# Performance work log

Hardware: AMD Instinct MI355X
Metric: run time of the kernel (lower is better)

Reference implementation:

```python
import jax, jax.numpy as jnp
import numpy as np

B, S, DIM = 32, 1, 2048
N_HEADS, N_KV = 32, 8
HEAD_DIM = DIM // N_HEADS  # 64
MAXB, MAXS = 32, 2048
START_POS = 2047
THETA = 10000.0  # precompute_freqs_cis called without theta -> llama default


def setup_inputs() -> dict:
    key = jax.random.key(0)
    ks = jax.random.split(key, 7)
    u = lambda k, s: jax.random.uniform(k, s, jnp.float32) * 0.02  # scaled torch.rand init
    return {
        "x": jax.random.normal(ks[0], (B, S, DIM), jnp.float32),
        "q_w": u(ks[1], (DIM, N_HEADS * HEAD_DIM)),
        "k_w": u(ks[2], (DIM, N_KV * HEAD_DIM)),
        "v_w": u(ks[3], (DIM, N_KV * HEAD_DIM)),
        "o_w": u(ks[4], (DIM, N_HEADS * HEAD_DIM)),
        "cache_k": jax.random.normal(ks[5], (MAXB, MAXS, N_KV, HEAD_DIM), jnp.float32) * 0.02,
        "cache_v": jax.random.normal(ks[6], (MAXB, MAXS, N_KV, HEAD_DIM), jnp.float32) * 0.02,
        "start_pos": START_POS,
    }


def _rope(x, cos, sin):
    # x: [B, S, H, D]; consecutive pairs (even, odd) form complex numbers (llama view_as_complex)
    xr, xi = x[..., 0::2], x[..., 1::2]
    out = jnp.stack([xr * cos - xi * sin, xr * sin + xi * cos], axis=-1)
    return out.reshape(x.shape)


def _attn_fwd(x, q_w, k_w, v_w, o_w, cache_k, cache_v, start_pos):
    B_, S_, _ = x.shape
    # fused_linear(x, W) == x @ W
    xq = (x @ q_w).reshape(B_, S_, N_HEADS, HEAD_DIM)
    xk = (x @ k_w).reshape(B_, S_, N_KV, HEAD_DIM)
    xv = (x @ v_w).reshape(B_, S_, N_KV, HEAD_DIM)

    # RoPE freqs for positions [start_pos, start_pos + S)
    inv = 1.0 / (THETA ** (jnp.arange(0, HEAD_DIM, 2, dtype=jnp.float32) / HEAD_DIM))
    t = jnp.arange(start_pos, start_pos + S_, dtype=jnp.float32)
    ang = t[:, None] * inv[None, :]                    # [S, D/2]
    cos = jnp.cos(ang)[None, :, None, :]               # [1, S, 1, D/2]
    sin = jnp.sin(ang)[None, :, None, :]
    xq = _rope(xq, cos, sin)
    xk = _rope(xk, cos, sin)

    # KV-cache append
    cache_k = jax.lax.dynamic_update_slice(cache_k, xk, (0, start_pos, 0, 0))
    cache_v = jax.lax.dynamic_update_slice(cache_v, xv, (0, start_pos, 0, 0))
    L = start_pos + S_
    keys = cache_k[:B_, :L].transpose(0, 2, 1, 3)      # [B, Hkv, L, D]
    vals = cache_v[:B_, :L].transpose(0, 2, 1, 3)

    # GQA attention; grouped einsum = repeat_kv without materializing copies
    rep = N_HEADS // N_KV
    q = xq.transpose(0, 2, 1, 3).reshape(B_, N_KV, rep, S_, HEAD_DIM)
    scores = jnp.einsum('bkrsd,bkld->bkrsl', q, keys) * (HEAD_DIM ** -0.5)
    p = jax.nn.softmax(scores, axis=-1)
    o = jnp.einsum('bkrsl,bkld->bkrsd', p, vals)
    o = o.reshape(B_, N_HEADS, S_, HEAD_DIM).transpose(0, 2, 1, 3).reshape(B_, S_, -1)
    return o @ o_w


def reference(x, q_w, k_w, v_w, o_w, cache_k, cache_v, start_pos):
    return _attn_fwd(x, q_w, k_w, v_w, o_w, cache_k, cache_v, start_pos)
```

## Files before the change

kernel.cpp:

```cpp
#include <hip/hip_runtime.h>
#include <hip/hip_bf16.h>
#include <math.h>

#define NQKV 3072
#define NS 8
#define SPL 256

__device__ __forceinline__ int read_sp(const int* spp) {
  if (!spp) return 2047;
  int raw = spp[0];
  if (raw >= 0 && raw < 2048) return raw;
  union { int i; float f; } u; u.i = raw;
  if (u.f >= 0.f && u.f < 2048.f) return (int)u.f;
  return 2047;
}

__global__ __launch_bounds__(256) void k_prep(const float* __restrict__ x,
                                              float* __restrict__ xt,
                                              float* __restrict__ rope,
                                              const int* __restrict__ spp) {
  int idx = blockIdx.x * 256 + threadIdx.x;
  int r = idx >> 11, k = idx & 2047;
  xt[k * 32 + r] = x[idx];
  if (blockIdx.x == 0 && threadIdx.x < 32) {
    int i = threadIdx.x;
    int sp = read_sp(spp);
    double freq = pow(10000.0, -(double)(2 * i) / 64.0);
    double ang = (double)sp * freq;
    double sd, cd; sincos(ang, &sd, &cd);
    rope[2 * i]     = (float)cd;
    rope[2 * i + 1] = (float)sd;
  }
}

__global__ __launch_bounds__(256) void k_qkv(const float* __restrict__ qw,
                                             const float* __restrict__ kw,
                                             const float* __restrict__ vw,
                                             const float* __restrict__ xt,
                                             float* __restrict__ part, int kc) {
  int colb = blockIdx.x, j = blockIdx.y;
  int n = colb * 256 + threadIdx.x;
  const float* w; int ldw, nn;
  if (colb < 8)       { w = qw; ldw = 2048; nn = n; }
  else if (colb < 10) { w = kw; ldw = 512;  nn = n - 2048; }
  else                { w = vw; ldw = 512;  nn = n - 2560; }
  int k0 = j * kc;
  const float* wp = w + (size_t)k0 * ldw + nn;
  float acc[32];
  #pragma unroll
  for (int r = 0; r < 32; r++) acc[r] = 0.f;
  #pragma unroll 8
  for (int kk = 0; kk < kc; kk++) {
    float wv = wp[(size_t)kk * ldw];
    const float* xr = xt + (size_t)(k0 + kk) * 32;
    #pragma unroll
    for (int r = 0; r < 32; r++) acc[r] = fmaf(xr[r], wv, acc[r]);
  }
  float* po = part + (size_t)j * 32 * NQKV + n;
  #pragma unroll
  for (int r = 0; r < 32; r++) po[(size_t)r * NQKV] = acc[r];
}

__global__ __launch_bounds__(256) void k_qred(const float* __restrict__ part,
                                              float* __restrict__ qred, int ks) {
  int col = blockIdx.x * 256 + threadIdx.x;
  int b = blockIdx.y;
  float s = 0.f;
  for (int j = 0; j < ks; j++) s += part[(size_t)(j * 32 + b) * NQKV + col];
  qred[(size_t)b * NQKV + col] = s;
}

__global__ __launch_bounds__(256) void k_attn_split(const float* __restrict__ ck,
                                                    const float* __restrict__ cv,
                                                    const float* __restrict__ qred,
                                                    const float* __restrict__ rope,
                                                    float* __restrict__ osplit,
                                                    float* __restrict__ msl,
                                                    const int* __restrict__ spp) {
  int h = blockIdx.x, b = blockIdx.y, s = blockIdx.z;
  int tid = threadIdx.x;
  int sp = read_sp(spp);

  __shared__ float qraw[384];
  __shared__ __align__(16) float qs[4][64];
  __shared__ __align__(16) float knew[64];
  __shared__ __align__(16) float vnew[64];
  __shared__ __align__(16) float sc[4][SPL];
  __shared__ float wredm[4][4];
  __shared__ float wred[4];
  __shared__ float mfin[4];
  __shared__ __align__(16) float opart[4][4][64];

  for (int i = tid; i < 384; i += 256) {
    int col;
    if (i < 256)      col = h * 256 + i;
    else if (i < 320) col = 2048 + h * 64 + (i - 256);
    else              col = 2560 + h * 64 + (i - 320);
    qraw[i] = qred[(size_t)b * NQKV + col];
  }
  __syncthreads();

  if (tid < 160) {
    int rr = tid >> 5, i = tid & 31;
    float cs = rope[2 * i], sn = rope[2 * i + 1];
    if (rr < 4) {
      float a = qraw[rr * 64 + 2 * i], bq = qraw[rr * 64 + 2 * i + 1];
      qs[rr][2 * i]     = (a * cs - bq * sn) * 0.125f;
      qs[rr][2 * i + 1] = (a * sn + bq * cs) * 0.125f;
    } else {
      float a = qraw[256 + 2 * i], bk = qraw[256 + 2 * i + 1];
      knew[2 * i]     = a * cs - bk * sn;
      knew[2 * i + 1] = a * sn + bk * cs;
    }
  } else if (tid < 224) {
    vnew[tid - 160] = qraw[320 + (tid - 160)];
  }
  __syncthreads();

  int w    = tid >> 6;
  int lane = tid & 63;
  int pp   = lane >> 4;
  int d4   = lane & 15;
  int base = s * SPL + w * 64;

  float4 qv0 = *(const float4*)&qs[0][d4 * 4];
  float4 qv1 = *(const float4*)&qs[1][d4 * 4];
  float4 qv2 = *(const float4*)&qs[2][d4 * 4];
  float4 qv3 = *(const float4*)&qs[3][d4 * 4];
  float4 kn4 = *(const float4*)&knew[d4 * 4];
  float4 vn4 = *(const float4*)&vnew[d4 * 4];

  const float* kb = ck + ((size_t)b * 2048 * 8 + h) * 64;
  float lm0 = -1e30f, lm1 = -1e30f, lm2 = -1e30f, lm3 = -1e30f;
  #pragma unroll
  for (int i = 0; i < 16; i++) {
    int p = base + i * 4 + pp;
    float4 k4 = *(const float4*)(kb + (size_t)p * 512 + d4 * 4);
    if (p == sp) k4 = kn4;
    float s0 = qv0.x * k4.x + qv0.y * k4.y + qv0.z * k4.z + qv0.w * k4.w;
    float s1 = qv1.x * k4.x + qv1.y * k4.y + qv1.z * k4.z + qv1.w * k4.w;
    float s2 = qv2.x * k4.x + qv2.y * k4.y + qv2.z * k4.z + qv2.w * k4.w;
    float s3 = qv3.x * k4.x + qv3.y * k4.y + qv3.z * k4.z + qv3.w * k4.w;
    #pragma unroll
    for (int off = 1; off <= 8; off <<= 1) {
      s0 += __shfl_xor(s0, off);
      s1 += __shfl_xor(s1, off);
      s2 += __shfl_xor(s2, off);
      s3 += __shfl_xor(s3, off);
    }
    lm0 = fmaxf(lm0, s0); lm1 = fmaxf(lm1, s1);
    lm2 = fmaxf(lm2, s2); lm3 = fmaxf(lm3, s3);
    float sv = (d4 == 0) ? s0 : (d4 == 1) ? s1 : (d4 == 2) ? s2 : s3;
    if (d4 < 4) sc[d4][w * 64 + i * 4 + pp] = sv;
  }
  lm0 = fmaxf(lm0, __shfl_xor(lm0, 16)); lm0 = fmaxf(lm0, __shfl_xor(lm0, 32));
  lm1 = fmaxf(lm1, __shfl_xor(lm1, 16)); lm1 = fmaxf(lm1, __shfl_xor(lm1, 32));
  lm2 = fmaxf(lm2, __shfl_xor(lm2, 16)); lm2 = fmaxf(lm2, __shfl_xor(lm2, 32));
  lm3 = fmaxf(lm3, __shfl_xor(lm3, 16)); lm3 = fmaxf(lm3, __shfl_xor(lm3, 32));
  if (lane == 0) {
    wredm[w][0] = lm0; wredm[w][1] = lm1; wredm[w][2] = lm2; wredm[w][3] = lm3;
  }
  __syncthreads();
  if (tid < 4)
    mfin[tid] = fmaxf(fmaxf(wredm[0][tid], wredm[1][tid]),
                      fmaxf(wredm[2][tid], wredm[3][tid]));
  __syncthreads();

  {
    int r = w, t = lane;
    float m = mfin[r];
    float lsum = 0.f;
    #pragma unroll
    for (int jj = 0; jj < 4; jj++) {
      float e = __expf(sc[r][jj * 64 + t] - m);
      lsum += e;
      sc[r][jj * 64 + t] = e;
    }
    #pragma unroll
    for (int off = 32; off > 0; off >>= 1) lsum += __shfl_xor(lsum, off);
    if (lane == 0) wred[r] = lsum;
  }
  __syncthreads();

  if (tid < 4) {
    size_t idx = (((size_t)(h * 32 + b) * NS + s) * 4 + tid) * 2;
    msl[idx]     = mfin[tid];
    msl[idx + 1] = wred[tid];
  }

  const float* vb = cv + ((size_t)b * 2048 * 8 + h) * 64;
  float4 a0 = {0,0,0,0}, a1 = {0,0,0,0}, a2 = {0,0,0,0}, a3 = {0,0,0,0};
  #pragma unroll
  for (int i = 0; i < 16; i++) {
    int p = base + i * 4 + pp;
    float4 v4 = *(const float4*)(vb + (size_t)p * 512 + d4 * 4);
    if (p == sp) v4 = vn4;
    int pl = w * 64 + i * 4 + pp;
    float e0 = sc[0][pl], e1 = sc[1][pl], e2 = sc[2][pl], e3 = sc[3][pl];
    a0.x = fmaf(e0, v4.x, a0.x); a0.y = fmaf(e0, v4.y, a0.y);
    a0.z = fmaf(e0, v4.z, a0.z); a0.w = fmaf(e0, v4.w, a0.w);
    a1.x = fmaf(e1, v4.x, a1.x); a1.y = fmaf(e1, v4.y, a1.y);
    a1.z = fmaf(e1, v4.z, a1.z); a1.w = fmaf(e1, v4.w, a1.w);
    a2.x = fmaf(e2, v4.x, a2.x); a2.y = fmaf(e2, v4.y, a2.y);
    a2.z = fmaf(e2, v4.z, a2.z); a2.w = fmaf(e2, v4.w, a2.w);
    a3.x = fmaf(e3, v4.x, a3.x); a3.y = fmaf(e3, v4.y, a3.y);
    a3.z = fmaf(e3, v4.z, a3.z); a3.w = fmaf(e3, v4.w, a3.w);
  }
  #pragma unroll
  for (int off = 16; off <= 32; off <<= 1) {
    a0.x += __shfl_xor(a0.x, off); a0.y += __shfl_xor(a0.y, off);
    a0.z += __shfl_xor(a0.z, off); a0.w += __shfl_xor(a0.w, off);
    a1.x += __shfl_xor(a1.x, off); a1.y += __shfl_xor(a1.y, off);
    a1.z += __shfl_xor(a1.z, off); a1.w += __shfl_xor(a1.w, off);
    a2.x += __shfl_xor(a2.x, off); a2.y += __shfl_xor(a2.y, off);
    a2.z += __shfl_xor(a2.z, off); a2.w += __shfl_xor(a2.w, off);
    a3.x += __shfl_xor(a3.x, off); a3.y += __shfl_xor(a3.y, off);
    a3.z += __shfl_xor(a3.z, off); a3.w += __shfl_xor(a3.w, off);
  }
  if (pp == 0) {
    *(float4*)&opart[w][0][d4 * 4] = a0;
    *(float4*)&opart[w][1][d4 * 4] = a1;
    *(float4*)&opart[w][2][d4 * 4] = a2;
    *(float4*)&opart[w][3][d4 * 4] = a3;
  }
  __syncthreads();
  {
    int rr = tid >> 6, dd = tid & 63;
    float o = opart[0][rr][dd] + opart[1][rr][dd] +
              opart[2][rr][dd] + opart[3][rr][dd];
    osplit[(((size_t)(h * 32 + b) * NS + s) * 4 + rr) * 64 + dd] = o;
  }
}

__global__ __launch_bounds__(256) void k_combine(const float* __restrict__ osplit,
                                                 const float* __restrict__ msl,
                                                 float* __restrict__ obt) {
  int h = blockIdx.x, b = blockIdx.y;
  int tid = threadIdx.x;
  int r = tid >> 6, d = tid & 63;
  float ml[NS], ll[NS];
  float m = -1e30f;
  #pragma unroll
  for (int s2 = 0; s2 < NS; s2++) {
    size_t idx = (((size_t)(h * 32 + b) * NS + s2) * 4 + r) * 2;
    ml[s2] = msl[idx]; ll[s2] = msl[idx + 1];
    m = fmaxf(m, ml[s2]);
  }
  float L = 0.f, o = 0.f;
  #pragma unroll
  for (int s2 = 0; s2 < NS; s2++) {
    float wgt = __expf(ml[s2] - m);
    L = fmaf(wgt, ll[s2], L);
    o = fmaf(wgt, osplit[(((size_t)(h * 32 + b) * NS + s2) * 4 + r) * 64 + d], o);
  }
  int col = (h * 4 + r) * 64 + d;
  obt[(size_t)col * 32 + b] = o / L;
}

__global__ __launch_bounds__(256) void k_oproj(const float* __restrict__ ow,
                                               const float* __restrict__ obt,
                                               float* __restrict__ part, int kc) {
  int colb = blockIdx.x, j = blockIdx.y;
  int n = colb * 256 + threadIdx.x;
  int k0 = j * kc;
  const float* wp = ow + (size_t)k0 * 2048 + n;
  float acc[32];
  #pragma unroll
  for (int r = 0; r < 32; r++) acc[r] = 0.f;
  #pragma unroll 8
  for (int kk = 0; kk < kc; kk++) {
    float wv = wp[(size_t)kk * 2048];
    const float* xr = obt + (size_t)(k0 + kk) * 32;
    #pragma unroll
    for (int r = 0; r < 32; r++) acc[r] = fmaf(xr[r], wv, acc[r]);
  }
  float* po = part + (size_t)j * 32 * 2048 + n;
  #pragma unroll
  for (int r = 0; r < 32; r++) po[(size_t)r * 2048] = acc[r];
}

__global__ __launch_bounds__(256) void k_finish(const float* __restrict__ part,
                                                float* __restrict__ out, int ks) {
  int idx = blockIdx.x * 256 + threadIdx.x;
  float s = 0.f;
  for (int j = 0; j < ks; j++) s += part[(size_t)j * 65536 + idx];
  out[idx] = s;
}

extern "C" void kernel_launch(void* const* d_in, const int* in_sizes, int n_in,
                              void* d_out, int out_size, void* d_ws, size_t ws_size,
                              hipStream_t stream) {
  const float* x  = (const float*)d_in[0];
  const float* qw = (const float*)d_in[1];
  const float* kw = (const float*)d_in[2];
  const float* vw = (const float*)d_in[3];
  const float* ow = (const float*)d_in[4];
  const float* ck = (const float*)d_in[5];
  const float* cv = (const float*)d_in[6];
  const int*   sp = (n_in >= 8) ? (const int*)d_in[7] : nullptr;

  const size_t FIXED = 65536 + 65536 + 98304 + 524288 + 16384 + 64;
  int ks = 1;
  {
    const int cands[4] = {16, 8, 4, 2};
    for (int i = 0; i < 4; i++) {
      if ((FIXED + (size_t)cands[i] * 98304) * 4 <= ws_size) { ks = cands[i]; break; }
    }
  }
  int kc = 2048 / ks;

  float* ws     = (float*)d_ws;
  float* xt     = ws;
  float* part   = xt + 65536;
  float* obt    = part + (size_t)ks * 98304;
  float* qred   = obt + 65536;
  float* osplit = qred + 98304;
  float* msl    = osplit + 524288;
  float* rope   = msl + 16384;
  float* part_out = part;

  k_prep      <<<256,              256, 0, stream>>>(x, xt, rope, sp);
  k_qkv       <<<dim3(12, ks),     256, 0, stream>>>(qw, kw, vw, xt, part, kc);
  k_qred      <<<dim3(12, 32),     256, 0, stream>>>(part, qred, ks);
  k_attn_split<<<dim3(8, 32, NS),  256, 0, stream>>>(ck, cv, qred, rope, osplit, msl, sp);
  k_combine   <<<dim3(8, 32),      256, 0, stream>>>(osplit, msl, obt);
  k_oproj     <<<dim3(8, ks),      256, 0, stream>>>(ow, obt, part_out, kc);
  k_finish    <<<256,              256, 0, stream>>>(part_out, (float*)d_out, ks);
}
```

Measured before the change: 391.3 us.

## Rework GEMV tiling with shared x tiles and per-batch attention blocks

The QKV and output projection kernels now give each thread two output columns, loaded as float2, and read activations from a shared-memory tile instead of global memory. The attention kernel is reorganised so one 512-thread block processes all 8 KV heads for a batch and sequence chunk, which makes each cache-row read contiguous across heads. The number of sequence splits doubles to 16 with 128 positions each, and the combine kernel is reindexed to match. The K-split count can reach 32, which adds partial-sum traffic and leaves fewer blocks in the column dimension.

Result: slower. 418.1 us (+6.8%).

```diff
diff --git a/kernel.cpp b/kernel.cpp
--- a/kernel.cpp
+++ b/kernel.cpp
@@ -3,8 +3,9 @@
 #include <math.h>
 
 #define NQKV 3072
-#define NS 8
-#define SPL 256
+#define NS 16
+#define SPL 128
+#define KT 128
 
 __device__ __forceinline__ int read_sp(const int* spp) {
   if (!spp) return 2047;
@@ -33,109 +34,116 @@
   }
 }
 
-__global__ __launch_bounds__(256) void k_qkv(const float* __restrict__ qw,
-                                             const float* __restrict__ kw,
-                                             const float* __restrict__ vw,
-                                             const float* __restrict__ xt,
-                                             float* __restrict__ part, int kc) {
-  int colb = blockIdx.x, j = blockIdx.y;
-  int n = colb * 256 + threadIdx.x;
-  const float* w; int ldw, nn;
-  if (colb < 8)       { w = qw; ldw = 2048; nn = n; }
-  else if (colb < 10) { w = kw; ldw = 512;  nn = n - 2048; }
-  else                { w = vw; ldw = 512;  nn = n - 2560; }
+__global__ __launch_bounds__(256) void k_qkv3(const float* __restrict__ qw,
+                                              const float* __restrict__ kw,
+                                              const float* __restrict__ vw,
+                                              const float* __restrict__ xt,
+                                              float* __restrict__ part, int kc) {
+  int colb = blockIdx.x, j = blockIdx.y, t = threadIdx.x;
+  const float* w; int ldw, col, outcol;
+  if (colb < 4)       { w = qw; ldw = 2048; col = colb * 512 + t * 2; outcol = col; }
+  else if (colb == 4) { w = kw; ldw = 512;  col = t * 2; outcol = 2048 + col; }
+  else                { w = vw; ldw = 512;  col = t * 2; outcol = 2560 + col; }
+  __shared__ __align__(16) float xs[KT][32];
   int k0 = j * kc;
-  const float* wp = w + (size_t)k0 * ldw + nn;
-  float acc[32];
-  #pragma unroll
-  for (int r = 0; r < 32; r++) acc[r] = 0.f;
-  #pragma unroll 8
-  for (int kk = 0; kk < kc; kk++) {
-    float wv = wp[(size_t)kk * ldw];
-    const float* xr = xt + (size_t)(k0 + kk) * 32;
-    #pragma unroll
-    for (int r = 0; r < 32; r++) acc[r] = fmaf(xr[r], wv, acc[r]);
-  }
-  float* po = part + (size_t)j * 32 * NQKV + n;
-  #pragma unroll
-  for (int r = 0; r < 32; r++) po[(size_t)r * NQKV] = acc[r];
+  float2 acc[32];
+  #pragma unroll
+  for (int r = 0; r < 32; r++) { acc[r].x = 0.f; acc[r].y = 0.f; }
+  for (int kt = 0; kt < kc; kt += KT) {
+    int ksz = (kc - kt < KT) ? (kc - kt) : KT;
+    __syncthreads();
+    for (int idx = t; idx < ksz * 32; idx += 256)
+      ((float*)xs)[idx] = xt[(size_t)(k0 + kt) * 32 + idx];
+    __syncthreads();
+    const float* wp = w + (size_t)(k0 + kt) * ldw + col;
+    #pragma unroll 2
+    for (int kk = 0; kk < ksz; kk++) {
+      float2 wv = *(const float2*)&wp[(size_t)kk * ldw];
+      #pragma unroll
+      for (int r4 = 0; r4 < 8; r4++) {
+        float4 xr = *(const float4*)&xs[kk][r4 * 4];
+        acc[r4*4+0].x = fmaf(xr.x, wv.x, acc[r4*4+0].x);
+        acc[r4*4+0].y = fmaf(xr.x, wv.y, acc[r4*4+0].y);
+        acc[r4*4+1].x = fmaf(xr.y, wv.x, acc[r4*4+1].x);
+        acc[r4*4+1].y = fmaf(xr.y, wv.y, acc[r4*4+1].y);
+        acc[r4*4+2].x = fmaf(xr.z, wv.x, acc[r4*4+2].x);
+        acc[r4*4+2].y = fmaf(xr.z, wv.y, acc[r4*4+2].y);
+        acc[r4*4+3].x = fmaf(xr.w, wv.x, acc[r4*4+3].x);
+        acc[r4*4+3].y = fmaf(xr.w, wv.y, acc[r4*4+3].y);
+      }
+    }
+  }
+  float* po = part + (size_t)j * (32 * NQKV) + outcol;
+  #pragma unroll
+  for (int r = 0; r < 32; r++) *(float2*)&po[(size_t)r * NQKV] = acc[r];
 }
 
 __global__ __launch_bounds__(256) void k_qred(const float* __restrict__ part,
-                                              float* __restrict__ qred, int ks) {
+                                              float* __restrict__ qred, int js) {
   int col = blockIdx.x * 256 + threadIdx.x;
   int b = blockIdx.y;
   float s = 0.f;
-  for (int j = 0; j < ks; j++) s += part[(size_t)(j * 32 + b) * NQKV + col];
+  for (int j = 0; j < js; j++) s += part[(size_t)j * (32 * NQKV) + (size_t)b * NQKV + col];
   qred[(size_t)b * NQKV + col] = s;
 }
 
-__global__ __launch_bounds__(256) void k_attn_split(const float* __restrict__ ck,
-                                                    const float* __restrict__ cv,
-                                                    const float* __restrict__ qred,
-                                                    const float* __restrict__ rope,
-                                                    float* __restrict__ osplit,
-                                                    float* __restrict__ msl,
-                                                    const int* __restrict__ spp) {
-  int h = blockIdx.x, b = blockIdx.y, s = blockIdx.z;
-  int tid = threadIdx.x;
+__global__ __launch_bounds__(512) void k_attn3(const float* __restrict__ ck,
+                                               const float* __restrict__ cv,
+                                               const float* __restrict__ qred,
+                                               const float* __restrict__ rope,
+                                               float* __restrict__ osplit,
+                                               float* __restrict__ msl,
+                                               const int* __restrict__ spp) {
+  int s = blockIdx.x, b = blockIdx.y, tid = threadIdx.x;
   int sp = read_sp(spp);
 
-  __shared__ float qraw[384];
-  __shared__ __align__(16) float qs[4][64];
-  __shared__ __align__(16) float knew[64];
-  __shared__ __align__(16) float vnew[64];
-  __shared__ __align__(16) float sc[4][SPL];
-  __shared__ float wredm[4][4];
-  __shared__ float wred[4];
-  __shared__ float mfin[4];
-  __shared__ __align__(16) float opart[4][4][64];
-
-  for (int i = tid; i < 384; i += 256) {
-    int col;
-    if (i < 256)      col = h * 256 + i;
-    else if (i < 320) col = 2048 + h * 64 + (i - 256);
-    else              col = 2560 + h * 64 + (i - 320);
-    qraw[i] = qred[(size_t)b * NQKV + col];
+  __shared__ __align__(16) float qs[8][4][64];
+  __shared__ __align__(16) float knew[8][64];
+  __shared__ __align__(16) float vnew[8][64];
+  __shared__ __align__(16) float sc[8][4][SPL + 4];
+  __shared__ __align__(16) float opart[4][8][4][64];
+
+  const float* qb = qred + (size_t)b * NQKV;
+
+  {
+    int pi = tid * 2;
+    #pragma unroll
+    for (int u = 0; u < 2; u++, pi++) {
+      int hq = pi >> 5, i = pi & 31;
+      float cs = rope[2 * i], sn = rope[2 * i + 1];
+      float a = qb[hq * 64 + 2 * i], bb = qb[hq * 64 + 2 * i + 1];
+      qs[hq >> 2][hq & 3][2 * i]     = (a * cs - bb * sn) * 0.125f;
+      qs[hq >> 2][hq & 3][2 * i + 1] = (a * sn + bb * cs) * 0.125f;
+    }
+    if (tid < 256) {
+      int h = tid >> 5, i = tid & 31;
+      float cs = rope[2 * i], sn = rope[2 * i + 1];
+      float a = qb[2048 + h * 64 + 2 * i], bb = qb[2048 + h * 64 + 2 * i + 1];
+      knew[h][2 * i]     = a * cs - bb * sn;
+      knew[h][2 * i + 1] = a * sn + bb * cs;
+    }
+    { int h = tid >> 6, d = tid & 63; vnew[h][d] = qb[2560 + h * 64 + d]; }
   }
   __syncthreads();
 
-  if (tid < 160) {
-    int rr = tid >> 5, i = tid & 31;
-    float cs = rope[2 * i], sn = rope[2 * i + 1];
-    if (rr < 4) {
-      float a = qraw[rr * 64 + 2 * i], bq = qraw[rr * 64 + 2 * i + 1];
-      qs[rr][2 * i]     = (a * cs - bq * sn) * 0.125f;
-      qs[rr][2 * i + 1] = (a * sn + bq * cs) * 0.125f;
-    } else {
-      float a = qraw[256 + 2 * i], bk = qraw[256 + 2 * i + 1];
-      knew[2 * i]     = a * cs - bk * sn;
-      knew[2 * i + 1] = a * sn + bk * cs;
-    }
-  } else if (tid < 224) {
-    vnew[tid - 160] = qraw[320 + (tid - 160)];
-  }
-  __syncthreads();
-
-  int w    = tid >> 6;
-  int lane = tid & 63;
-  int pp   = lane >> 4;
-  int d4   = lane & 15;
-  int base = s * SPL + w * 64;
-
-  float4 qv0 = *(const float4*)&qs[0][d4 * 4];
-  float4 qv1 = *(const float4*)&qs[1][d4 * 4];
-  float4 qv2 = *(const float4*)&qs[2][d4 * 4];
-  float4 qv3 = *(const float4*)&qs[3][d4 * 4];
-  float4 kn4 = *(const float4*)&knew[d4 * 4];
-  float4 vn4 = *(const float4*)&vnew[d4 * 4];
-
-  const float* kb = ck + ((size_t)b * 2048 * 8 + h) * 64;
-  float lm0 = -1e30f, lm1 = -1e30f, lm2 = -1e30f, lm3 = -1e30f;
-  #pragma unroll
-  for (int i = 0; i < 16; i++) {
-    int p = base + i * 4 + pp;
-    float4 k4 = *(const float4*)(kb + (size_t)p * 512 + d4 * 4);
+  int w = tid >> 6, lane = tid & 63;
+  int w2 = w >> 1, half = w & 1;
+  int hh2 = lane >> 4, d4 = lane & 15;
+  int h = half * 4 + hh2;
+
+  float4 qv0 = *(const float4*)&qs[h][0][d4 * 4];
+  float4 qv1 = *(const float4*)&qs[h][1][d4 * 4];
+  float4 qv2 = *(const float4*)&qs[h][2][d4 * 4];
+  float4 qv3 = *(const float4*)&qs[h][3][d4 * 4];
+  float4 kn4 = *(const float4*)&knew[h][d4 * 4];
+  float4 vn4 = *(const float4*)&vnew[h][d4 * 4];
+
+  const float* kb = ck + (size_t)b * 2048 * 512 + half * 256 + lane * 4;
+  int pbase = s * SPL + w2;
+  #pragma unroll 4
+  for (int i = 0; i < 32; i++) {
+    int p = pbase + i * 4;
+    float4 k4 = *(const float4*)(kb + (size_t)p * 512);
     if (p == sp) k4 = kn4;
     float s0 = qv0.x * k4.x + qv0.y * k4.y + qv0.z * k4.z + qv0.w * k4.w;
     float s1 = qv1.x * k4.x + qv1.y * k4.y + qv1.z * k4.z + qv1.w * k4.w;
@@ -148,55 +156,39 @@
       s2 += __shfl_xor(s2, off);
       s3 += __shfl_xor(s3, off);
     }
-    lm0 = fmaxf(lm0, s0); lm1 = fmaxf(lm1, s1);
-    lm2 = fmaxf(lm2, s2); lm3 = fmaxf(lm3, s3);
     float sv = (d4 == 0) ? s0 : (d4 == 1) ? s1 : (d4 == 2) ? s2 : s3;
-    if (d4 < 4) sc[d4][w * 64 + i * 4 + pp] = sv;
-  }
-  lm0 = fmaxf(lm0, __shfl_xor(lm0, 16)); lm0 = fmaxf(lm0, __shfl_xor(lm0, 32));
-  lm1 = fmaxf(lm1, __shfl_xor(lm1, 16)); lm1 = fmaxf(lm1, __shfl_xor(lm1, 32));
-  lm2 = fmaxf(lm2, __shfl_xor(lm2, 16)); lm2 = fmaxf(lm2, __shfl_xor(lm2, 32));
-  lm3 = fmaxf(lm3, __shfl_xor(lm3, 16)); lm3 = fmaxf(lm3, __shfl_xor(lm3, 32));
-  if (lane == 0) {
-    wredm[w][0] = lm0; wredm[w][1] = lm1; wredm[w][2] = lm2; wredm[w][3] = lm3;
+    if (d4 < 4) sc[h][d4][p - s * SPL] = sv;
   }
   __syncthreads();
-  if (tid < 4)
-    mfin[tid] = fmaxf(fmaxf(wredm[0][tid], wredm[1][tid]),
-                      fmaxf(wredm[2][tid], wredm[3][tid]));
+
+  #pragma unroll
+  for (int q = 0; q < 4; q++) {
+    int row = w * 4 + q, rh = row >> 2, rr = row & 3;
+    float2 v01 = *(const float2*)&sc[rh][rr][lane * 2];
+    float m = fmaxf(v01.x, v01.y);
+    #pragma unroll
+    for (int off = 1; off <= 32; off <<= 1) m = fmaxf(m, __shfl_xor(m, off));
+    float e0 = __expf(v01.x - m), e1 = __expf(v01.y - m);
+    sc[rh][rr][lane * 2] = e0; sc[rh][rr][lane * 2 + 1] = e1;
+    float l = e0 + e1;
+    #pragma unroll
+    for (int off = 1; off <= 32; off <<= 1) l += __shfl_xor(l, off);
+    if (lane == 0) {
+      size_t mi = (((size_t)b * NS + s) * 32 + row) * 2;
+      msl[mi] = m; msl[mi + 1] = l;
+    }
+  }
   __syncthreads();
 
-  {
-    int r = w, t = lane;
-    float m = mfin[r];
-    float lsum = 0.f;
-    #pragma unroll
-    for (int jj = 0; jj < 4; jj++) {
-      float e = __expf(sc[r][jj * 64 + t] - m);
-      lsum += e;
-      sc[r][jj * 64 + t] = e;
-    }
-    #pragma unroll
-    for (int off = 32; off > 0; off >>= 1) lsum += __shfl_xor(lsum, off);
-    if (lane == 0) wred[r] = lsum;
-  }
-  __syncthreads();
-
-  if (tid < 4) {
-    size_t idx = (((size_t)(h * 32 + b) * NS + s) * 4 + tid) * 2;
-    msl[idx]     = mfin[tid];
-    msl[idx + 1] = wred[tid];
-  }
-
-  const float* vb = cv + ((size_t)b * 2048 * 8 + h) * 64;
+  const float* vb = cv + (size_t)b * 2048 * 512 + half * 256 + lane * 4;
   float4 a0 = {0,0,0,0}, a1 = {0,0,0,0}, a2 = {0,0,0,0}, a3 = {0,0,0,0};
-  #pragma unroll
-  for (int i = 0; i < 16; i++) {
-    int p = base + i * 4 + pp;
-    float4 v4 = *(const float4*)(vb + (size_t)p * 512 + d4 * 4);
+  #pragma unroll 4
+  for (int i = 0; i < 32; i++) {
+    int p = pbase + i * 4;
+    float4 v4 = *(const float4*)(vb + (size_t)p * 512);
     if (p == sp) v4 = vn4;
-    int pl = w * 64 + i * 4 + pp;
-    float e0 = sc[0][pl], e1 = sc[1][pl], e2 = sc[2][pl], e3 = sc[3][pl];
+    int pl = p - s * SPL;
+    float e0 = sc[h][0][pl], e1 = sc[h][1][pl], e2 = sc[h][2][pl], e3 = sc[h][3][pl];
     a0.x = fmaf(e0, v4.x, a0.x); a0.y = fmaf(e0, v4.y, a0.y);
     a0.z = fmaf(e0, v4.z, a0.z); a0.w = fmaf(e0, v4.w, a0.w);
     a1.x = fmaf(e1, v4.x, a1.x); a1.y = fmaf(e1, v4.y, a1.y);
@@ -206,84 +198,92 @@
     a3.x = fmaf(e3, v4.x, a3.x); a3.y = fmaf(e3, v4.y, a3.y);
     a3.z = fmaf(e3, v4.z, a3.z); a3.w = fmaf(e3, v4.w, a3.w);
   }
-  #pragma unroll
-  for (int off = 16; off <= 32; off <<= 1) {
-    a0.x += __shfl_xor(a0.x, off); a0.y += __shfl_xor(a0.y, off);
-    a0.z += __shfl_xor(a0.z, off); a0.w += __shfl_xor(a0.w, off);
-    a1.x += __shfl_xor(a1.x, off); a1.y += __shfl_xor(a1.y, off);
-    a1.z += __shfl_xor(a1.z, off); a1.w += __shfl_xor(a1.w, off);
-    a2.x += __shfl_xor(a2.x, off); a2.y += __shfl_xor(a2.y, off);
-    a2.z += __shfl_xor(a2.z, off); a2.w += __shfl_xor(a2.w, off);
-    a3.x += __shfl_xor(a3.x, off); a3.y += __shfl_xor(a3.y, off);
-    a3.z += __shfl_xor(a3.z, off); a3.w += __shfl_xor(a3.w, off);
-  }
-  if (pp == 0) {
-    *(float4*)&opart[w][0][d4 * 4] = a0;
-    *(float4*)&opart[w][1][d4 * 4] = a1;
-    *(float4*)&opart[w][2][d4 * 4] = a2;
-    *(float4*)&opart[w][3][d4 * 4] = a3;
-  }
+  *(float4*)&opart[w2][h][0][d4 * 4] = a0;
+  *(float4*)&opart[w2][h][1][d4 * 4] = a1;
+  *(float4*)&opart[w2][h][2][d4 * 4] = a2;
+  *(float4*)&opart[w2][h][3][d4 * 4] = a3;
   __syncthreads();
-  {
-    int rr = tid >> 6, dd = tid & 63;
-    float o = opart[0][rr][dd] + opart[1][rr][dd] +
-              opart[2][rr][dd] + opart[3][rr][dd];
-    osplit[(((size_t)(h * 32 + b) * NS + s) * 4 + rr) * 64 + dd] = o;
-  }
-}
-
-__global__ __launch_bounds__(256) void k_combine(const float* __restrict__ osplit,
-                                                 const float* __restrict__ msl,
-                                                 float* __restrict__ obt) {
-  int h = blockIdx.x, b = blockIdx.y;
-  int tid = threadIdx.x;
-  int r = tid >> 6, d = tid & 63;
-  float ml[NS], ll[NS];
+
+  for (int e = tid; e < 2048; e += 512) {
+    int eh = e >> 8, er = (e >> 6) & 3, ed = e & 63;
+    float o = opart[0][eh][er][ed] + opart[1][eh][er][ed] +
+              opart[2][eh][er][ed] + opart[3][eh][er][ed];
+    osplit[(((size_t)b * NS + s) * 32 + eh * 4 + er) * 64 + ed] = o;
+  }
+}
+
+__global__ __launch_bounds__(256) void k_combine3(const float* __restrict__ osplit,
+                                                  const float* __restrict__ msl,
+                                                  float* __restrict__ obt) {
+  int b = blockIdx.x, g = blockIdx.y, t = threadIdx.x;
+  int hq = g * 8 + (t >> 5);
+  int d0 = (t & 31) * 2;
+  float ms[NS], ls[NS];
   float m = -1e30f;
   #pragma unroll
-  for (int s2 = 0; s2 < NS; s2++) {
-    size_t idx = (((size_t)(h * 32 + b) * NS + s2) * 4 + r) * 2;
-    ml[s2] = msl[idx]; ll[s2] = msl[idx + 1];
-    m = fmaxf(m, ml[s2]);
-  }
-  float L = 0.f, o = 0.f;
-  #pragma unroll
-  for (int s2 = 0; s2 < NS; s2++) {
-    float wgt = __expf(ml[s2] - m);
-    L = fmaf(wgt, ll[s2], L);
-    o = fmaf(wgt, osplit[(((size_t)(h * 32 + b) * NS + s2) * 4 + r) * 64 + d], o);
-  }
-  int col = (h * 4 + r) * 64 + d;
-  obt[(size_t)col * 32 + b] = o / L;
-}
-
-__global__ __launch_bounds__(256) void k_oproj(const float* __restrict__ ow,
-                                               const float* __restrict__ obt,
-                                               float* __restrict__ part, int kc) {
-  int colb = blockIdx.x, j = blockIdx.y;
-  int n = colb * 256 + threadIdx.x;
+  for (int s = 0; s < NS; s++) {
+    size_t mi = (((size_t)b * NS + s) * 32 + hq) * 2;
+    ms[s] = msl[mi]; ls[s] = msl[mi + 1];
+    m = fmaxf(m, ms[s]);
+  }
+  float L = 0.f, o0 = 0.f, o1 = 0.f;
+  #pragma unroll
+  for (int s = 0; s < NS; s++) {
+    float wgt = __expf(ms[s] - m);
+    L = fmaf(wgt, ls[s], L);
+    const float* op = osplit + (((size_t)b * NS + s) * 32 + hq) * 64 + d0;
+    o0 = fmaf(wgt, op[0], o0);
+    o1 = fmaf(wgt, op[1], o1);
+  }
+  float invL = 1.f / L;
+  obt[(size_t)(hq * 64 + d0) * 32 + b]     = o0 * invL;
+  obt[(size_t)(hq * 64 + d0 + 1) * 32 + b] = o1 * invL;
+}
+
+__global__ __launch_bounds__(256) void k_oproj3(const float* __restrict__ ow,
+                                                const float* __restrict__ obt,
+                                                float* __restrict__ part, int kc) {
+  int colb = blockIdx.x, j = blockIdx.y, t = threadIdx.x;
+  int col = colb * 512 + t * 2;
+  __shared__ __align__(16) float xs[KT][32];
   int k0 = j * kc;
-  const float* wp = ow + (size_t)k0 * 2048 + n;
-  float acc[32];
-  #pragma unroll
-  for (int r = 0; r < 32; r++) acc[r] = 0.f;
-  #pragma unroll 8
-  for (int kk = 0; kk < kc; kk++) {
-    float wv = wp[(size_t)kk * 2048];
-    const float* xr = obt + (size_t)(k0 + kk) * 32;
-    #pragma unroll
-    for (int r = 0; r < 32; r++) acc[r] = fmaf(xr[r], wv, acc[r]);
-  }
-  float* po = part + (size_t)j * 32 * 2048 + n;
-  #pragma unroll
-  for (int r = 0; r < 32; r++) po[(size_t)r * 2048] = acc[r];
+  float2 acc[32];
+  #pragma unroll
+  for (int r = 0; r < 32; r++) { acc[r].x = 0.f; acc[r].y = 0.f; }
+  for (int kt = 0; kt < kc; kt += KT) {
+    int ksz = (kc - kt < KT) ? (kc - kt) : KT;
+    __syncthreads();
+    for (int idx = t; idx < ksz * 32; idx += 256)
+      ((float*)xs)[idx] = obt[(size_t)(k0 + kt) * 32 + idx];
+    __syncthreads();
+    const float* wp = ow + (size_t)(k0 + kt) * 2048 + col;
+    #pragma unroll 2
+    for (int kk = 0; kk < ksz; kk++) {
+      float2 wv = *(const float2*)&wp[(size_t)kk * 2048];
+      #pragma unroll
+      for (int r4 = 0; r4 < 8; r4++) {
+        float4 xr = *(const float4*)&xs[kk][r4 * 4];
+        acc[r4*4+0].x = fmaf(xr.x, wv.x, acc[r4*4+0].x);
+        acc[r4*4+0].y = fmaf(xr.x, wv.y, acc[r4*4+0].y);
+        acc[r4*4+1].x = fmaf(xr.y, wv.x, acc[r4*4+1].x);
+        acc[r4*4+1].y = fmaf(xr.y, wv.y, acc[r4*4+1].y);
+        acc[r4*4+2].x = fmaf(xr.z, wv.x, acc[r4*4+2].x);
+        acc[r4*4+2].y = fmaf(xr.z, wv.y, acc[r4*4+2].y);
+        acc[r4*4+3].x = fmaf(xr.w, wv.x, acc[r4*4+3].x);
+        acc[r4*4+3].y = fmaf(xr.w, wv.y, acc[r4*4+3].y);
+      }
+    }
+  }
+  float* po = part + (size_t)j * 65536 + col;
+  #pragma unroll
+  for (int r = 0; r < 32; r++) *(float2*)&po[(size_t)r * 2048] = acc[r];
 }
 
 __global__ __launch_bounds__(256) void k_finish(const float* __restrict__ part,
-                                                float* __restrict__ out, int ks) {
+                                                float* __restrict__ out, int js) {
   int idx = blockIdx.x * 256 + threadIdx.x;
   float s = 0.f;
-  for (int j = 0; j < ks; j++) s += part[(size_t)j * 65536 + idx];
+  for (int j = 0; j < js; j++) s += part[(size_t)j * 65536 + idx];
   out[idx] = s;
 }
 
@@ -299,31 +299,30 @@
   const float* cv = (const float*)d_in[6];
   const int*   sp = (n_in >= 8) ? (const int*)d_in[7] : nullptr;
 
-  const size_t FIXED = 65536 + 65536 + 98304 + 524288 + 16384 + 64;
-  int ks = 1;
+  const size_t FIXED = 65536 + 65536 + 98304 + 1048576 + 32768 + 64;
+  int js = 2;
   {
-    const int cands[4] = {16, 8, 4, 2};
-    for (int i = 0; i < 4; i++) {
-      if ((FIXED + (size_t)cands[i] * 98304) * 4 <= ws_size) { ks = cands[i]; break; }
-    }
-  }
-  int kc = 2048 / ks;
+    const int cands[5] = {32, 16, 8, 4, 2};
+    for (int i = 0; i < 5; i++) {
+      if ((FIXED + (size_t)cands[i] * 98304) * 4 <= ws_size) { js = cands[i]; break; }
+    }
+  }
+  int kc = 2048 / js;
 
   float* ws     = (float*)d_ws;
   float* xt     = ws;
   float* part   = xt + 65536;
-  float* obt    = part + (size_t)ks * 98304;
+  float* obt    = part + (size_t)js * 98304;
   float* qred   = obt + 65536;
   float* osplit = qred + 98304;
-  float* msl    = osplit + 524288;
-  float* rope   = msl + 16384;
-  float* part_out = part;
-
-  k_prep      <<<256,              256, 0, stream>>>(x, xt, rope, sp);
-  k_qkv       <<<dim3(12, ks),     256, 0, stream>>>(qw, kw, vw, xt, part, kc);
-  k_qred      <<<dim3(12, 32),     256, 0, stream>>>(part, qred, ks);
-  k_attn_split<<<dim3(8, 32, NS),  256, 0, stream>>>(ck, cv, qred, rope, osplit, msl, sp);
-  k_combine   <<<dim3(8, 32),      256, 0, stream>>>(osplit, msl, obt);
-  k_oproj     <<<dim3(8, ks),      256, 0, stream>>>(ow, obt, part_out, kc);
-  k_finish    <<<256,              256, 0, stream>>>(part_out, (float*)d_out, ks);
-}
+  float* msl    = osplit + 1048576;
+  float* rope   = msl + 32768;
+
+  k_prep    <<<256,             256, 0, stream>>>(x, xt, rope, sp);
+  k_qkv3    <<<dim3(6, js),     256, 0, stream>>>(qw, kw, vw, xt, part, kc);
+  k_qred    <<<dim3(12, 32),    256, 0, stream>>>(part, qred, js);
+  k_attn3   <<<dim3(NS, 32),    512, 0, stream>>>(ck, cv, qred, rope, osplit, msl, sp);
+  k_combine3<<<dim3(32, 4),     256, 0, stream>>>(osplit, msl, obt);
+  k_oproj3  <<<dim3(4, js),     256, 0, stream>>>(ow, obt, part, kc);
+  k_finish  <<<256,             256, 0, stream>>>(part, (float*)d_out, js);
+}
```
